# Performance work log

Measured on AMD Instinct MI355X. Metric: run time of the kernel, lower is better.

Reference implementation:

```python
import jax, jax.numpy as jnp
import numpy as np

B, N, H, SD, MAXS, MINS = 16, 1024, 64, 64, 16, 2
ETA = 0.01

def setup_inputs() -> dict:
    key = jax.random.key(0)
    ks = jax.random.split(key, 8)
    rn = lambda k, shape, sc=1.0: jax.random.normal(k, shape, dtype=jnp.float32) * sc
    return {
        "gene_state": rn(ks[0], (B, N, H)),
        "coherent_state": rn(ks[1], (B, N, H)),
        "state_embeddings": rn(ks[2], (MAXS, SD), 0.1),
        "gamma_base": jnp.ones((N,), jnp.float32) * 0.1,
        "env_w1": rn(ks[3], (H, 32), 0.1), "env_b1": jnp.zeros((32,), jnp.float32),
        "env_w2": rn(ks[4], (32, 1), 0.1), "env_b2": jnp.zeros((1,), jnp.float32),
        "omega_w1": rn(ks[5], (H, 32), 0.1), "omega_b1": jnp.zeros((32,), jnp.float32),
        "omega_w2": rn(ks[6], (32, 1), 0.1), "omega_b2": jnp.zeros((1,), jnp.float32),
        "Hmat": rn(ks[7], (N, N), 0.1),
    }

def reference(gene_state, coherent_state, state_embeddings, gamma_base,
              env_w1, env_b1, env_w2, env_b2,
              omega_w1, omega_b1, omega_w2, omega_b2, Hmat):
    # --- CellularStateBank: cosine-similarity softmax over active states ---
    cell = gene_state.mean(axis=1)                                   # [B, H]
    active = state_embeddings[:MINS]                                 # [MINS, SD]
    cn = cell / jnp.clip(jnp.linalg.norm(cell, axis=-1, keepdims=True), 1e-12)
    sn = active / jnp.clip(jnp.linalg.norm(active, axis=-1, keepdims=True), 1e-12)
    state_probs = jax.nn.softmax(cn @ sn.T / 0.1, axis=-1)           # [B, MINS]

    # --- DecoherenceLayer: env-coupled collapse toward classical mean ---
    h1 = jax.nn.silu(gene_state @ env_w1 + env_b1)                   # [B, N, 32]
    env = jax.nn.sigmoid((h1 @ env_w2 + env_b2)[..., 0])             # [B, N]
    gamma = jax.nn.sigmoid(gamma_base) * (1.0 + env)                 # [B, N]
    classical = jnp.mean(gene_state, axis=-1, keepdims=True)         # [B, N, 1]
    ge = gamma[..., None]
    decohered = (1.0 - ge) * coherent_state + ge * classical         # [B, N, H]

    # --- GreensFunctionLayer: batched complex resolvent inversion ---
    o1 = jax.nn.silu(gene_state @ omega_w1 + omega_b1)               # [B, N, 32]
    omega = (o1 @ omega_w2 + omega_b2)[..., 0]                       # [B, N]
    omega_mean = omega.mean(axis=1)                                  # [B]
    H_sym = 0.5 * (Hmat + Hmat.T)
    I = jnp.eye(N, dtype=jnp.complex64)
    w = omega_mean.astype(jnp.complex64) + jnp.complex64(1j * ETA)   # [B]
    R = w[:, None, None] * I - H_sym.astype(jnp.complex64)           # [B, N, N]
    propagator = jnp.abs(jnp.linalg.inv(R))                          # [B, N, N]

    return state_probs, decohered, gamma, propagator
```

## Files before the change

kernel.cpp:

```cpp
#include <hip/hip_runtime.h>
#include <hip/hip_bf16.h>

constexpr int kB  = 16;
constexpr int kN  = 1024;
constexpr int kH  = 64;
constexpr int kNB = 64;
constexpr int kNT = 16;

typedef float f4 __attribute__((ext_vector_type(4)));

__device__ __forceinline__ float2 cmul(float2 a, float2 b) {
  return make_float2(a.x * b.x - a.y * b.y, a.x * b.y + a.y * b.x);
}
__device__ __forceinline__ float2 cfma(float2 a, float2 b, float2 acc) {
  acc.x = fmaf(a.x, b.x, fmaf(-a.y, b.y, acc.x));
  acc.y = fmaf(a.x, b.y, fmaf( a.y, b.x, acc.y));
  return acc;
}
__device__ __forceinline__ float2 cnfma(float2 a, float2 b, float2 acc) {
  acc.x = fmaf(-a.x, b.x, fmaf( a.y, b.y, acc.x));
  acc.y = fmaf(-a.x, b.y, fmaf(-a.y, b.x, acc.y));
  return acc;
}
__device__ __forceinline__ float2 cinv(float2 p) {
  float d = 1.0f / (p.x * p.x + p.y * p.y);
  return make_float2(p.x * d, -p.y * d);
}
__device__ __forceinline__ float2 csel(bool c, float2 a, float2 b) {
  return c ? a : b;
}

struct TileLds {
  f4 Ar[64][9];
  f4 Ai[64][9];
  f4 Br[32][17];
  f4 Bi[32][17];
};

struct PivSmem {
  float2 P[kNB][kNB + 1];
  float2 Cst[kNB][4];
  float2 Rst[4][kNB];
};

union FusedSmem {
  TileLds tile;
  PivSmem piv;
};

union UpdSmem {
  TileLds tile;
  float2  M[64][66];
};

__device__ __forceinline__ void stage_tiles(
    TileLds& L, int t,
    const float* __restrict__ Agr, const float* __restrict__ Agi, int astride,
    const float* __restrict__ Bgr, const float* __restrict__ Bgi, int bstride)
{
  #pragma unroll
  for (int q = 0; q < 2; ++q) {
    int e = q * 256 + t;
    int ra = e >> 3, ca = e & 7;
    L.Ar[ra][ca] = *(const f4*)(Agr + (size_t)ra * astride + ca * 4);
    L.Ai[ra][ca] = *(const f4*)(Agi + (size_t)ra * astride + ca * 4);
    int rb = e >> 4, cb = e & 15;
    L.Br[rb][cb] = *(const f4*)(Bgr + (size_t)rb * bstride + cb * 4);
    L.Bi[rb][cb] = *(const f4*)(Bgi + (size_t)rb * bstride + cb * 4);
  }
}

__device__ __forceinline__ void prefetch_regs(
    int t,
    const float* __restrict__ Agr, const float* __restrict__ Agi, int astride,
    const float* __restrict__ Bgr, const float* __restrict__ Bgi, int bstride,
    f4 (&sar)[2], f4 (&sai)[2], f4 (&sbr)[2], f4 (&sbi)[2])
{
  #pragma unroll
  for (int q = 0; q < 2; ++q) {
    int e = q * 256 + t;
    int ra = e >> 3, ca = e & 7;
    sar[q] = *(const f4*)(Agr + (size_t)ra * astride + ca * 4);
    sai[q] = *(const f4*)(Agi + (size_t)ra * astride + ca * 4);
    int rb = e >> 4, cb = e & 15;
    sbr[q] = *(const f4*)(Bgr + (size_t)rb * bstride + cb * 4);
    sbi[q] = *(const f4*)(Bgi + (size_t)rb * bstride + cb * 4);
  }
}

__device__ __forceinline__ void regs_to_lds(
    TileLds& L, int t,
    const f4 (&sar)[2], const f4 (&sai)[2],
    const f4 (&sbr)[2], const f4 (&sbi)[2])
{
  #pragma unroll
  for (int q = 0; q < 2; ++q) {
    int e = q * 256 + t;
    int ra = e >> 3, ca = e & 7;
    L.Ar[ra][ca] = sar[q]; L.Ai[ra][ca] = sai[q];
    int rb = e >> 4, cb = e & 15;
    L.Br[rb][cb] = sbr[q]; L.Bi[rb][cb] = sbi[q];
  }
}

__device__ __forceinline__ void cgemm_tile(
    const TileLds& L, int r0, int c0q, float (&cr)[4][4], float (&ci)[4][4])
{
  #pragma unroll 2
  for (int mq = 0; mq < 8; ++mq) {
    f4 ar[4], ai[4];
    #pragma unroll
    for (int i = 0; i < 4; ++i) {
      ar[i] = L.Ar[r0 + i][mq];
      ai[i] = L.Ai[r0 + i][mq];
    }
    #pragma unroll
    for (int mm = 0; mm < 4; ++mm) {
      f4 br = L.Br[mq * 4 + mm][c0q];
      f4 bi = L.Bi[mq * 4 + mm][c0q];
      #pragma unroll
      for (int i = 0; i < 4; ++i) {
        float a_r = ar[i][mm], a_i = ai[i][mm];
        #pragma unroll
        for (int j = 0; j < 4; ++j) {
          cr[i][j] = fmaf(a_r, br[j], fmaf(-a_i, bi[j], cr[i][j]));
          ci[i][j] = fmaf(a_r, bi[j], fmaf( a_i, br[j], ci[i][j]));
        }
      }
    }
  }
}

__global__ __launch_bounds__(64) void rows_kernel(
    const float* __restrict__ gene, const float* __restrict__ coh,
    const float* __restrict__ gbase,
    const float* __restrict__ ew1, const float* __restrict__ eb1,
    const float* __restrict__ ew2, const float* __restrict__ eb2,
    const float* __restrict__ ow1, const float* __restrict__ ob1,
    const float* __restrict__ ow2, const float* __restrict__ ob2,
    float* __restrict__ out_dec, float* __restrict__ out_gamma,
    float* __restrict__ ws_omega)
{
  int row = blockIdx.x;
  int n   = row & (kN - 1);
  int t   = threadIdx.x;
  float g = gene[(size_t)row * kH + t];

  float s = g;
  #pragma unroll
  for (int off = 32; off >= 1; off >>= 1) s += __shfl_xor(s, off);
  float classical = s * (1.0f / kH);

  bool isEnv = t < 32;
  int  j     = isEnv ? t : (t - 32);
  const float* w1 = isEnv ? ew1 : ow1;
  float acc = isEnv ? eb1[j] : ob1[j];
  #pragma unroll
  for (int h = 0; h < kH; ++h) {
    float gh = __shfl(g, h);
    acc = fmaf(gh, w1[h * 32 + j], acc);
  }
  float sl   = acc * (1.0f / (1.0f + expf(-acc)));
  float term = sl * (isEnv ? ew2[j] : ow2[j]);
  #pragma unroll
  for (int off = 16; off >= 1; off >>= 1) term += __shfl_xor(term, off);
  float env_sum = __shfl(term, 0);
  float om_sum  = __shfl(term, 32);

  float env   = 1.0f / (1.0f + expf(-(env_sum + eb2[0])));
  float gamma = (1.0f / (1.0f + expf(-gbase[n]))) * (1.0f + env);

  float dec = (1.0f - gamma) * coh[(size_t)row * kH + t] + gamma * classical;
  out_dec[(size_t)row * kH + t] = dec;
  if (t == 0)  out_gamma[row] = gamma;
  if (t == 63) ws_omega[row]  = om_sum + ob2[0];
}

__global__ __launch_bounds__(256) void probs_kernel(
    const float* __restrict__ gene, const float* __restrict__ emb,
    float* __restrict__ outp)
{
  __shared__ float red[256];
  __shared__ float cell[64];
  int b = blockIdx.x, t = threadIdx.x;
  int h = t & 63, seg = t >> 6;
  float s = 0.0f;
  for (int n = seg * 256; n < seg * 256 + 256; ++n)
    s += gene[((size_t)b * kN + n) * kH + h];
  red[t] = s;
  __syncthreads();
  if (t < 64) cell[t] = (red[t] + red[t + 64] + red[t + 128] + red[t + 192]) * (1.0f / kN);
  __syncthreads();
  if (t == 0) {
    float nc = 0.0f;
    for (int x = 0; x < 64; ++x) nc += cell[x] * cell[x];
    nc = fmaxf(sqrtf(nc), 1e-12f);
    float l[2];
    for (int s2 = 0; s2 < 2; ++s2) {
      float ne = 0.0f, dot = 0.0f;
      for (int x = 0; x < 64; ++x) { float e = emb[s2 * 64 + x]; ne += e * e; }
      ne = fmaxf(sqrtf(ne), 1e-12f);
      for (int x = 0; x < 64; ++x) dot += (cell[x] / nc) * (emb[s2 * 64 + x] / ne);
      l[s2] = dot * 10.0f;
    }
    float m  = fmaxf(l[0], l[1]);
    float e0 = expf(l[0] - m), e1 = expf(l[1] - m);
    outp[b * 2 + 0] = e0 / (e0 + e1);
    outp[b * 2 + 1] = e1 / (e0 + e1);
  }
}

__global__ __launch_bounds__(256) void omean_kernel(
    const float* __restrict__ om, float* __restrict__ omm)
{
  __shared__ float red[256];
  int b = blockIdx.x, t = threadIdx.x;
  float s = om[b * kN + t] + om[b * kN + t + 256] + om[b * kN + t + 512] + om[b * kN + t + 768];
  red[t] = s;
  __syncthreads();
  for (int off = 128; off >= 1; off >>= 1) {
    if (t < off) red[t] += red[t + off];
    __syncthreads();
  }
  if (t == 0) omm[b] = red[0] * (1.0f / kN);
}

__global__ __launch_bounds__(256) void hs_kernel(
    const float* __restrict__ Hm, float* __restrict__ Hs)
{
  int idx = blockIdx.x * 256 + threadIdx.x;
  int i = idx >> 10, j = idx & 1023;
  Hs[idx] = 0.5f * (Hm[i * kN + j] + Hm[j * kN + i]);
}

__global__ __launch_bounds__(256) void build_kernel(
    const float* __restrict__ Hs, const float* __restrict__ omm,
    float* __restrict__ Are, float* __restrict__ Aim, int b0)
{
  int bb = blockIdx.y;
  int e = blockIdx.x * 256 + threadIdx.x;
  int i = e >> 8, j4 = e & 255;
  float wr = omm[b0 + bb];
  f4 h = *(const f4*)(Hs + (size_t)e * 4);
  f4 re, im;
  #pragma unroll
  for (int c = 0; c < 4; ++c) {
    bool d = (j4 * 4 + c == i);
    re[c] = (d ? wr : 0.0f) - h[c];
    im[c] = d ? 0.01f : 0.0f;
  }
  *(f4*)(Are + (size_t)bb * kN * kN + (size_t)e * 4) = re;
  *(f4*)(Aim + (size_t)bb * kN * kN + (size_t)e * 4) = im;
}

__device__ void pivotinv_dev(
    PivSmem& S,
    const float* __restrict__ Are, const float* __restrict__ Aim,
    float* __restrict__ Pro, float* __restrict__ Pio, int kstep, int bb, int t)
{
  size_t base = (size_t)bb * kN * kN + (size_t)(kstep * kNB) * kN + kstep * kNB;

  #pragma unroll
  for (int q = 0; q < 16; ++q) {
    int e = q * 256 + t;
    int r = e >> 6, c = e & 63;
    S.P[r][c] = make_float2(Are[base + (size_t)r * kN + c],
                            Aim[base + (size_t)r * kN + c]);
  }
  __syncthreads();

  const int c = t & 63;
  const int w = t >> 6;
  const int cq = c & 3;

  for (int ps = 0; ps < 16; ++ps) {
    const int p0 = ps * 4;
    S.Cst[t >> 2][t & 3]  = S.P[t >> 2][p0 + (t & 3)];
    S.Rst[t >> 6][t & 63] = S.P[p0 + (t >> 6)][t & 63];
    __syncthreads();

    float2 E[4][4];
    #pragma unroll
    for (int r = 0; r < 4; ++r)
      #pragma unroll
      for (int q = 0; q < 4; ++q) E[r][q] = S.Rst[r][p0 + q];
    #pragma unroll
    for (int s4 = 0; s4 < 4; ++s4) {
      float2 ip = cinv(E[s4][s4]);
      #pragma unroll
      for (int cc = 0; cc < 4; ++cc)
        if (cc != s4) E[s4][cc] = cmul(E[s4][cc], ip);
      #pragma unroll
      for (int i = 0; i < 4; ++i)
        if (i != s4) {
          float2 f = E[i][s4];
          #pragma unroll
          for (int cc = 0; cc < 4; ++cc)
            if (cc != s4) E[i][cc] = cnfma(f, E[s4][cc], E[i][cc]);
          E[i][s4] = cmul(make_float2(-f.x, -f.y), ip);
        }
      E[s4][s4] = ip;
    }

    float2 Rp[4];
    #pragma unroll
    for (int r = 0; r < 4; ++r) {
      float2 acc = cmul(E[r][0], S.Rst[0][c]);
      acc = cfma(E[r][1], S.Rst[1][c], acc);
      acc = cfma(E[r][2], S.Rst[2][c], acc);
      acc = cfma(E[r][3], S.Rst[3][c], acc);
      Rp[r] = acc;
    }

    const bool cinP = (c >= p0) && (c < p0 + 4);
    float2 Ecol[4];
    #pragma unroll
    for (int r = 0; r < 4; ++r) {
      float2 a = csel(cq & 1, E[r][1], E[r][0]);
      float2 b = csel(cq & 1, E[r][3], E[r][2]);
      Ecol[r] = csel(cq & 2, b, a);
    }
    float2 ra  = csel(w & 1, Rp[1], Rp[0]);
    float2 rb  = csel(w & 1, Rp[3], Rp[2]);
    float2 Rpw = csel(w & 2, rb, ra);
    float2 ea  = csel(w & 1, Ecol[1], Ecol[0]);
    float2 eb  = csel(w & 1, Ecol[3], Ecol[2]);
    float2 Ecw = csel(w & 2, eb, ea);
    float2 inPval = csel(cinP, Ecw, Rpw);

    #pragma unroll
    for (int qq = 0; qq < 16; ++qq) {
      int i = w + 4 * qq;
      const f4* fp = (const f4*)(&S.Cst[i][0]);
      f4 f01 = fp[0], f23 = fp[1];
      float2 f0 = make_float2(f01.x, f01.y), f1 = make_float2(f01.z, f01.w);
      float2 f2 = make_float2(f23.x, f23.y), f3 = make_float2(f23.z, f23.w);
      float2 old = S.P[i][c];
      float2 g = old;
      g = cnfma(f0, Rp[0], g);
      g = cnfma(f1, Rp[1], g);
      g = cnfma(f2, Rp[2], g);
      g = cnfma(f3, Rp[3], g);
      float2 cp = cmul(f0, Ecol[0]);
      cp = cfma(f1, Ecol[1], cp);
      cp = cfma(f2, Ecol[2], cp);
      cp = cfma(f3, Ecol[3], cp);
      cp.x = -cp.x; cp.y = -cp.y;
      float2 other = csel(cinP, cp, g);
      float2 res   = csel(qq == ps, inPval, other);
      S.P[i][c] = res;
    }
    __syncthreads();
  }

  int pbase = bb * kNB * kNB;
  #pragma unroll
  for (int q = 0; q < 16; ++q) {
    int e = q * 256 + t;
    int r = e >> 6, cc = e & 63;
    float2 v  = S.P[r][cc];
    float2 vt = S.P[cc][r];
    Pro[pbase + e] = 0.5f * (v.x + vt.x);
    Pio[pbase + e] = 0.5f * (v.y + vt.y);
  }
}

__global__ __launch_bounds__(256) void pivotinv_kernel(
    const float* __restrict__ Are, const float* __restrict__ Aim,
    float* __restrict__ Pro, float* __restrict__ Pio, int kstep)
{
  __shared__ PivSmem S;
  pivotinv_dev(S, Are, Aim, Pro, Pio, kstep, blockIdx.x, threadIdx.x);
}

__device__ void rowfix_dev(
    TileLds& L,
    float* __restrict__ Are, float* __restrict__ Aim,
    const float* __restrict__ Pr, const float* __restrict__ Pi,
    int kstep, int ct, int bb, int t)
{
  int pbase = bb * kNB * kNB;
  size_t rb = (size_t)bb * kN * kN + (size_t)(kstep * kNB) * kN + ct * kNB;
  if (ct == kstep) {
    for (int e = t; e < kNB * kNB / 4; e += 256) {
      int r = e >> 4, c4 = e & 15;
      *(f4*)(Are + rb + (size_t)r * kN + c4 * 4) = *(const f4*)(Pr + pbase + e * 4);
      *(f4*)(Aim + rb + (size_t)r * kN + c4 * 4) = *(const f4*)(Pi + pbase + e * 4);
    }
    return;
  }
  float cr[4][4] = {}, ci[4][4] = {};
  int r0 = (t >> 4) * 4, c0q = t & 15;

  stage_tiles(L, t, Pr + pbase, Pi + pbase, kNB,
              Are + rb, Aim + rb, kN);
  __syncthreads();

  f4 sar[2], sai[2], sbr[2], sbi[2];
  prefetch_regs(t, Pr + pbase + 32, Pi + pbase + 32, kNB,
                Are + rb + (size_t)32 * kN, Aim + rb + (size_t)32 * kN, kN,
                sar, sai, sbr, sbi);
  cgemm_tile(L, r0, c0q, cr, ci);
  __syncthreads();

  regs_to_lds(L, t, sar, sai, sbr, sbi);
  __syncthreads();
  cgemm_tile(L, r0, c0q, cr, ci);

  #pragma unroll
  for (int i = 0; i < 4; ++i) {
    size_t idx = rb + (size_t)(r0 + i) * kN + c0q * 4;
    *(f4*)(Are + idx) = (f4){cr[i][0], cr[i][1], cr[i][2], cr[i][3]};
    *(f4*)(Aim + idx) = (f4){ci[i][0], ci[i][1], ci[i][2], ci[i][3]};
  }
}

__global__ __launch_bounds__(256) void rowpiv_kernel(
    float* __restrict__ Are, float* __restrict__ Aim,
    const float* __restrict__ Prc, const float* __restrict__ Pic,
    float* __restrict__ Prn, float* __restrict__ Pin, int kstep)
{
  __shared__ FusedSmem S;
  int x = blockIdx.x, bb = blockIdx.y, t = threadIdx.x;
  if (x == kNT) {
    pivotinv_dev(S.piv, Are, Aim, Prn, Pin, kstep + 1, bb, t);
    return;
  }
  rowfix_dev(S.tile, Are, Aim, Prc, Pic, kstep, x, bb, t);
}

__global__ __launch_bounds__(256) void colgemm_kernel(
    float* __restrict__ Are, float* __restrict__ Aim,
    const float* __restrict__ Pr, const float* __restrict__ Pi, int kstep)
{
  int rt = blockIdx.x;
  if (rt == kstep) return;
  int bb = blockIdx.y, t = threadIdx.x;
  size_t abase = (size_t)bb * kN * kN + (size_t)(rt * kNB) * kN + kstep * kNB;
  int pbase = bb * kNB * kNB;
  __shared__ TileLds L;
  float cr[4][4] = {}, ci[4][4] = {};
  int r0 = (t >> 4) * 4, c0q = t & 15;

  stage_tiles(L, t, Are + abase, Aim + abase, kN,
              Pr + pbase, Pi + pbase, kNB);
  __syncthreads();

  f4 sar[2], sai[2], sbr[2], sbi[2];
  prefetch_regs(t, Are + abase + 32, Aim + abase + 32, kN,
                Pr + pbase + 32 * kNB, Pi + pbase + 32 * kNB, kNB,
                sar, sai, sbr, sbi);
  cgemm_tile(L, r0, c0q, cr, ci);
  __syncthreads();

  regs_to_lds(L, t, sar, sai, sbr, sbi);
  __syncthreads();
  cgemm_tile(L, r0, c0q, cr, ci);

  #pragma unroll
  for (int i = 0; i < 4; ++i) {
    size_t idx = abase + (size_t)(r0 + i) * kN + c0q * 4;
    *(f4*)(Are + idx) = (f4){-cr[i][0], -cr[i][1], -cr[i][2], -cr[i][3]};
    *(f4*)(Aim + idx) = (f4){-ci[i][0], -ci[i][1], -ci[i][2], -ci[i][3]};
  }
}

__global__ __launch_bounds__(256) void update_kernel(
    float* __restrict__ Are, float* __restrict__ Aim, int kstep)
{
  int idx = blockIdx.x;
  int bb  = blockIdx.y;
  int t   = threadIdx.x;
  int a = (int)((sqrtf(8.0f * (float)idx + 1.0f) - 1.0f) * 0.5f);
  while ((a + 1) * (a + 2) / 2 <= idx) ++a;
  while (a * (a + 1) / 2 > idx) --a;
  int b = idx - a * (a + 1) / 2;
  int rt = a + (a >= kstep);
  int ct = b + (b >= kstep);

  size_t NNb     = (size_t)bb * kN * kN;
  size_t colbase = NNb + (size_t)(rt * kNB) * kN + kstep * kNB;
  size_t rowbase = NNb + (size_t)(kstep * kNB) * kN + ct * kNB;
  size_t cb      = NNb + (size_t)(rt * kNB) * kN + ct * kNB;
  __shared__ UpdSmem S;
  float cr[4][4] = {}, ci[4][4] = {};
  int r0 = (t >> 4) * 4, c0q = t & 15;

  stage_tiles(S.tile, t, Are + colbase, Aim + colbase, kN,
              Are + rowbase, Aim + rowbase, kN);
  __syncthreads();

  f4 sar[2], sai[2], sbr[2], sbi[2];
  prefetch_regs(t, Are + colbase + 32, Aim + colbase + 32, kN,
                Are + rowbase + (size_t)32 * kN,
                Aim + rowbase + (size_t)32 * kN, kN,
                sar, sai, sbr, sbi);
  cgemm_tile(S.tile, r0, c0q, cr, ci);
  __syncthreads();

  regs_to_lds(S.tile, t, sar, sai, sbr, sbi);
  __syncthreads();
  cgemm_tile(S.tile, r0, c0q, cr, ci);

  f4 vr4[4], vi4[4];
  #pragma unroll
  for (int i = 0; i < 4; ++i) {
    size_t gidx = cb + (size_t)(r0 + i) * kN + c0q * 4;
    f4 vr = *(const f4*)(Are + gidx);
    f4 vi = *(const f4*)(Aim + gidx);
    vr += (f4){cr[i][0], cr[i][1], cr[i][2], cr[i][3]};
    vi += (f4){ci[i][0], ci[i][1], ci[i][2], ci[i][3]};
    *(f4*)(Are + gidx) = vr;
    *(f4*)(Aim + gidx) = vi;
    vr4[i] = vr; vi4[i] = vi;
  }

  if (rt != ct) {
    float eps = ((rt < kstep) == (ct < kstep)) ? 1.0f : -1.0f;
    __syncthreads();
    #pragma unroll
    for (int i = 0; i < 4; ++i)
      #pragma unroll
      for (int j = 0; j < 4; ++j)
        S.M[c0q * 4 + j][r0 + i] =
            make_float2(eps * vr4[i][j], eps * vi4[i][j]);
    __syncthreads();
    size_t mb = NNb + (size_t)(ct * kNB) * kN + rt * kNB;
    #pragma unroll
    for (int q = 0; q < 4; ++q) {
      int e = q * 256 + t;
      int r = e >> 4, c4 = e & 15;
      float2 m0 = S.M[r][c4 * 4 + 0], m1 = S.M[r][c4 * 4 + 1];
      float2 m2 = S.M[r][c4 * 4 + 2], m3 = S.M[r][c4 * 4 + 3];
      *(f4*)(Are + mb + (size_t)r * kN + c4 * 4) = (f4){m0.x, m1.x, m2.x, m3.x};
      *(f4*)(Aim + mb + (size_t)r * kN + c4 * 4) = (f4){m0.y, m1.y, m2.y, m3.y};
    }
  }
}

__global__ __launch_bounds__(256) void abs_kernel(
    const float* __restrict__ Are, const float* __restrict__ Aim,
    float* __restrict__ outp)
{
  size_t e = (size_t)blockIdx.x * 256 + threadIdx.x;
  f4 re = *(const f4*)(Are + e * 4);
  f4 im = *(const f4*)(Aim + e * 4);
  f4 o;
  #pragma unroll
  for (int c = 0; c < 4; ++c) o[c] = sqrtf(re[c] * re[c] + im[c] * im[c]);
  *(f4*)(outp + e * 4) = o;
}

extern "C" void kernel_launch(void* const* d_in, const int* in_sizes, int n_in,
                              void* d_out, int out_size, void* d_ws, size_t ws_size,
                              hipStream_t stream)
{
  const float* gene  = (const float*)d_in[0];
  const float* coh   = (const float*)d_in[1];
  const float* emb   = (const float*)d_in[2];
  const float* gbase = (const float*)d_in[3];
  const float* ew1   = (const float*)d_in[4];
  const float* eb1   = (const float*)d_in[5];
  const float* ew2   = (const float*)d_in[6];
  const float* eb2   = (const float*)d_in[7];
  const float* ow1   = (const float*)d_in[8];
  const float* ob1   = (const float*)d_in[9];
  const float* ow2   = (const float*)d_in[10];
  const float* ob2   = (const float*)d_in[11];
  const float* Hm    = (const float*)d_in[12];

  float* out       = (float*)d_out;
  float* out_probs = out;
  float* out_dec   = out + 32;
  float* out_gamma = out + 32 + 1048576;
  float* out_prop  = out + 32 + 1048576 + 16384;

  const size_t NN      = (size_t)kN * kN;
  const size_t PB      = (size_t)kNB * kNB;
  const size_t perB    = 2 * NN + 4 * PB;
  const size_t fixedF  = NN + (size_t)kB * kN + 16;
  size_t availF = ws_size / 4;
  int chunk = 1;
  if (availF > fixedF + perB) {
    size_t c = (availF - fixedF) / perB;
    chunk = (int)(c > 16 ? 16 : c);
    if (chunk < 1) chunk = 1;
  }

  float* Are  = (float*)d_ws;
  float* Aim  = Are + (size_t)chunk * NN;
  float* Pr0  = Aim + (size_t)chunk * NN;
  float* Pi0  = Pr0 + (size_t)chunk * PB;
  float* Pr1  = Pi0 + (size_t)chunk * PB;
  float* Pi1  = Pr1 + (size_t)chunk * PB;
  float* Hs   = Pi1 + (size_t)chunk * PB;
  float* wsom = Hs  + NN;
  float* womm = wsom + (size_t)kB * kN;

  rows_kernel<<<kB * kN, 64, 0, stream>>>(gene, coh, gbase, ew1, eb1, ew2, eb2,
                                          ow1, ob1, ow2, ob2,
                                          out_dec, out_gamma, wsom);
  probs_kernel<<<kB, 256, 0, stream>>>(gene, emb, out_probs);
  omean_kernel<<<kB, 256, 0, stream>>>(wsom, womm);
  hs_kernel<<<(kN * kN) / 256, 256, 0, stream>>>(Hm, Hs);

  for (int b0 = 0; b0 < kB; b0 += chunk) {
    int c = (b0 + chunk <= kB) ? chunk : (kB - b0);
    build_kernel<<<dim3((kN * kN) / 1024, c), 256, 0, stream>>>(Hs, womm, Are, Aim, b0);
    pivotinv_kernel<<<c, 256, 0, stream>>>(Are, Aim, Pr0, Pi0, 0);
    for (int k = 0; k < kNT; ++k) {
      float* Prc = (k & 1) ? Pr1 : Pr0;
      float* Pic = (k & 1) ? Pi1 : Pi0;
      float* Prn = (k & 1) ? Pr0 : Pr1;
      float* Pin = (k & 1) ? Pi0 : Pi1;
      colgemm_kernel<<<dim3(kNT, c), 256, 0, stream>>>(Are, Aim, Prc, Pic, k);
      update_kernel<<<dim3(120, c), 256, 0, stream>>>(Are, Aim, k);
      int gx = (k < kNT - 1) ? (kNT + 1) : kNT;
      rowpiv_kernel<<<dim3(gx, c), 256, 0, stream>>>(Are, Aim, Prc, Pic, Prn, Pin, k);
    }
    abs_kernel<<<c * (kN * kN / 1024), 256, 0, stream>>>(
        Are, Aim, out_prop + (size_t)b0 * NN);
  }
}
```

Before: 2.359 ms.

## Overlap next pivot inversion with trailing update and split probs reduction

Restructures the blocked Gauss-Jordan step schedule. The diagonal-tile update for the next pivot now runs first in its own tiny kernel. The next pivot-block inversion is then fused into the trailing-update launch, with its pair index skipped, so it runs concurrently with the bulk update rather than alongside the row fix. Row fixing becomes its own kernel. Separately, the per-batch cell mean reduction is split into a 16-way parallel partial-sum kernel plus a small finalize kernel to use more CUs. This adds one launch per step and an extra workspace buffer.

Result: slower. 3.199 ms (+35.6%).

```diff
diff --git a/kernel.cpp b/kernel.cpp
--- a/kernel.cpp
+++ b/kernel.cpp
@@ -43,14 +43,10 @@
   float2 Rst[4][kNB];
 };
 
-union FusedSmem {
-  TileLds tile;
-  PivSmem piv;
-};
-
-union UpdSmem {
+union UpdPivSmem {
   TileLds tile;
   float2  M[64][66];
+  PivSmem piv;
 };
 
 __device__ __forceinline__ void stage_tiles(
@@ -176,20 +172,32 @@
   if (t == 63) ws_omega[row]  = om_sum + ob2[0];
 }
 
-__global__ __launch_bounds__(256) void probs_kernel(
-    const float* __restrict__ gene, const float* __restrict__ emb,
+__global__ __launch_bounds__(256) void probs1_kernel(
+    const float* __restrict__ gene, float* __restrict__ prt)
+{
+  __shared__ float red[256];
+  int b = blockIdx.x, s = blockIdx.y, t = threadIdx.x;
+  int h = t & 63, q = t >> 6;
+  const float* gp = gene + ((size_t)b * kN + s * 64 + q * 16) * kH + h;
+  float sum = 0.0f;
+  #pragma unroll
+  for (int i = 0; i < 16; ++i) sum += gp[(size_t)i * kH];
+  red[t] = sum;
+  __syncthreads();
+  if (t < 64)
+    prt[(b * 16 + s) * 64 + t] = red[t] + red[t + 64] + red[t + 128] + red[t + 192];
+}
+
+__global__ __launch_bounds__(64) void probs2_kernel(
+    const float* __restrict__ prt, const float* __restrict__ emb,
     float* __restrict__ outp)
 {
-  __shared__ float red[256];
   __shared__ float cell[64];
   int b = blockIdx.x, t = threadIdx.x;
-  int h = t & 63, seg = t >> 6;
   float s = 0.0f;
-  for (int n = seg * 256; n < seg * 256 + 256; ++n)
-    s += gene[((size_t)b * kN + n) * kH + h];
-  red[t] = s;
-  __syncthreads();
-  if (t < 64) cell[t] = (red[t] + red[t + 64] + red[t + 128] + red[t + 192]) * (1.0f / kN);
+  #pragma unroll
+  for (int i = 0; i < 16; ++i) s += prt[(b * 16 + i) * 64 + t];
+  cell[t] = s * (1.0f / kN);
   __syncthreads();
   if (t == 0) {
     float nc = 0.0f;
@@ -373,62 +381,6 @@
   pivotinv_dev(S, Are, Aim, Pro, Pio, kstep, blockIdx.x, threadIdx.x);
 }
 
-__device__ void rowfix_dev(
-    TileLds& L,
-    float* __restrict__ Are, float* __restrict__ Aim,
-    const float* __restrict__ Pr, const float* __restrict__ Pi,
-    int kstep, int ct, int bb, int t)
-{
-  int pbase = bb * kNB * kNB;
-  size_t rb = (size_t)bb * kN * kN + (size_t)(kstep * kNB) * kN + ct * kNB;
-  if (ct == kstep) {
-    for (int e = t; e < kNB * kNB / 4; e += 256) {
-      int r = e >> 4, c4 = e & 15;
-      *(f4*)(Are + rb + (size_t)r * kN + c4 * 4) = *(const f4*)(Pr + pbase + e * 4);
-      *(f4*)(Aim + rb + (size_t)r * kN + c4 * 4) = *(const f4*)(Pi + pbase + e * 4);
-    }
-    return;
-  }
-  float cr[4][4] = {}, ci[4][4] = {};
-  int r0 = (t >> 4) * 4, c0q = t & 15;
-
-  stage_tiles(L, t, Pr + pbase, Pi + pbase, kNB,
-              Are + rb, Aim + rb, kN);
-  __syncthreads();
-
-  f4 sar[2], sai[2], sbr[2], sbi[2];
-  prefetch_regs(t, Pr + pbase + 32, Pi + pbase + 32, kNB,
-                Are + rb + (size_t)32 * kN, Aim + rb + (size_t)32 * kN, kN,
-                sar, sai, sbr, sbi);
-  cgemm_tile(L, r0, c0q, cr, ci);
-  __syncthreads();
-
-  regs_to_lds(L, t, sar, sai, sbr, sbi);
-  __syncthreads();
-  cgemm_tile(L, r0, c0q, cr, ci);
-
-  #pragma unroll
-  for (int i = 0; i < 4; ++i) {
-    size_t idx = rb + (size_t)(r0 + i) * kN + c0q * 4;
-    *(f4*)(Are + idx) = (f4){cr[i][0], cr[i][1], cr[i][2], cr[i][3]};
-    *(f4*)(Aim + idx) = (f4){ci[i][0], ci[i][1], ci[i][2], ci[i][3]};
-  }
-}
-
-__global__ __launch_bounds__(256) void rowpiv_kernel(
-    float* __restrict__ Are, float* __restrict__ Aim,
-    const float* __restrict__ Prc, const float* __restrict__ Pic,
-    float* __restrict__ Prn, float* __restrict__ Pin, int kstep)
-{
-  __shared__ FusedSmem S;
-  int x = blockIdx.x, bb = blockIdx.y, t = threadIdx.x;
-  if (x == kNT) {
-    pivotinv_dev(S.piv, Are, Aim, Prn, Pin, kstep + 1, bb, t);
-    return;
-  }
-  rowfix_dev(S.tile, Are, Aim, Prc, Pic, kstep, x, bb, t);
-}
-
 __global__ __launch_bounds__(256) void colgemm_kernel(
     float* __restrict__ Are, float* __restrict__ Aim,
     const float* __restrict__ Pr, const float* __restrict__ Pi, int kstep)
@@ -465,12 +417,10 @@
   }
 }
 
-__global__ __launch_bounds__(256) void update_kernel(
-    float* __restrict__ Are, float* __restrict__ Aim, int kstep)
-{
-  int idx = blockIdx.x;
-  int bb  = blockIdx.y;
-  int t   = threadIdx.x;
+__device__ void update_pair_dev(
+    UpdPivSmem& S, float* __restrict__ Are, float* __restrict__ Aim,
+    int kstep, int idx, int bb, int t)
+{
   int a = (int)((sqrtf(8.0f * (float)idx + 1.0f) - 1.0f) * 0.5f);
   while ((a + 1) * (a + 2) / 2 <= idx) ++a;
   while (a * (a + 1) / 2 > idx) --a;
@@ -482,7 +432,6 @@
   size_t colbase = NNb + (size_t)(rt * kNB) * kN + kstep * kNB;
   size_t rowbase = NNb + (size_t)(kstep * kNB) * kN + ct * kNB;
   size_t cb      = NNb + (size_t)(rt * kNB) * kN + ct * kNB;
-  __shared__ UpdSmem S;
   float cr[4][4] = {}, ci[4][4] = {};
   int r0 = (t >> 4) * 4, c0q = t & 15;
 
@@ -535,6 +484,71 @@
       *(f4*)(Are + mb + (size_t)r * kN + c4 * 4) = (f4){m0.x, m1.x, m2.x, m3.x};
       *(f4*)(Aim + mb + (size_t)r * kN + c4 * 4) = (f4){m0.y, m1.y, m2.y, m3.y};
     }
+  }
+}
+
+__global__ __launch_bounds__(256) void updiag_kernel(
+    float* __restrict__ Are, float* __restrict__ Aim, int kstep)
+{
+  __shared__ UpdPivSmem S;
+  int idxd = kstep * (kstep + 1) / 2 + kstep;
+  update_pair_dev(S, Are, Aim, kstep, idxd, blockIdx.y, threadIdx.x);
+}
+
+__global__ __launch_bounds__(256) void updpiv_kernel(
+    float* __restrict__ Are, float* __restrict__ Aim,
+    float* __restrict__ Prn, float* __restrict__ Pin,
+    int kstep, int skipidx, int withpiv)
+{
+  __shared__ UpdPivSmem S;
+  int x = blockIdx.x, bb = blockIdx.y, t = threadIdx.x;
+  if (withpiv && x == (int)gridDim.x - 1) {
+    pivotinv_dev(S.piv, Are, Aim, Prn, Pin, kstep + 1, bb, t);
+    return;
+  }
+  int idx = x + ((skipidx >= 0 && x >= skipidx) ? 1 : 0);
+  update_pair_dev(S, Are, Aim, kstep, idx, bb, t);
+}
+
+__global__ __launch_bounds__(256) void rowfix_kernel(
+    float* __restrict__ Are, float* __restrict__ Aim,
+    const float* __restrict__ Pr, const float* __restrict__ Pi, int kstep)
+{
+  int ct = blockIdx.x, bb = blockIdx.y, t = threadIdx.x;
+  int pbase = bb * kNB * kNB;
+  size_t rb = (size_t)bb * kN * kN + (size_t)(kstep * kNB) * kN + ct * kNB;
+  if (ct == kstep) {
+    for (int e = t; e < kNB * kNB / 4; e += 256) {
+      int r = e >> 4, c4 = e & 15;
+      *(f4*)(Are + rb + (size_t)r * kN + c4 * 4) = *(const f4*)(Pr + pbase + e * 4);
+      *(f4*)(Aim + rb + (size_t)r * kN + c4 * 4) = *(const f4*)(Pi + pbase + e * 4);
+    }
+    return;
+  }
+  __shared__ TileLds L;
+  float cr[4][4] = {}, ci[4][4] = {};
+  int r0 = (t >> 4) * 4, c0q = t & 15;
+
+  stage_tiles(L, t, Pr + pbase, Pi + pbase, kNB,
+              Are + rb, Aim + rb, kN);
+  __syncthreads();
+
+  f4 sar[2], sai[2], sbr[2], sbi[2];
+  prefetch_regs(t, Pr + pbase + 32, Pi + pbase + 32, kNB,
+                Are + rb + (size_t)32 * kN, Aim + rb + (size_t)32 * kN, kN,
+                sar, sai, sbr, sbi);
+  cgemm_tile(L, r0, c0q, cr, ci);
+  __syncthreads();
+
+  regs_to_lds(L, t, sar, sai, sbr, sbi);
+  __syncthreads();
+  cgemm_tile(L, r0, c0q, cr, ci);
+
+  #pragma unroll
+  for (int i = 0; i < 4; ++i) {
+    size_t idx = rb + (size_t)(r0 + i) * kN + c0q * 4;
+    *(f4*)(Are + idx) = (f4){cr[i][0], cr[i][1], cr[i][2], cr[i][3]};
+    *(f4*)(Aim + idx) = (f4){ci[i][0], ci[i][1], ci[i][2], ci[i][3]};
   }
 }
 
@@ -578,7 +592,7 @@
   const size_t NN      = (size_t)kN * kN;
   const size_t PB      = (size_t)kNB * kNB;
   const size_t perB    = 2 * NN + 4 * PB;
-  const size_t fixedF  = NN + (size_t)kB * kN + 16;
+  const size_t fixedF  = NN + (size_t)kB * kN + 16 + (size_t)kB * 16 * 64;
   size_t availF = ws_size / 4;
   int chunk = 1;
   if (availF > fixedF + perB) {
@@ -596,11 +610,13 @@
   float* Hs   = Pi1 + (size_t)chunk * PB;
   float* wsom = Hs  + NN;
   float* womm = wsom + (size_t)kB * kN;
+  float* prt  = womm + 16;
 
   rows_kernel<<<kB * kN, 64, 0, stream>>>(gene, coh, gbase, ew1, eb1, ew2, eb2,
                                           ow1, ob1, ow2, ob2,
                                           out_dec, out_gamma, wsom);
-  probs_kernel<<<kB, 256, 0, stream>>>(gene, emb, out_probs);
+  probs1_kernel<<<dim3(kB, 16), 256, 0, stream>>>(gene, prt);
+  probs2_kernel<<<kB, 64, 0, stream>>>(prt, emb, out_probs);
   omean_kernel<<<kB, 256, 0, stream>>>(wsom, womm);
   hs_kernel<<<(kN * kN) / 256, 256, 0, stream>>>(Hm, Hs);
 
@@ -614,9 +630,16 @@
       float* Prn = (k & 1) ? Pr0 : Pr1;
       float* Pin = (k & 1) ? Pi0 : Pi1;
       colgemm_kernel<<<dim3(kNT, c), 256, 0, stream>>>(Are, Aim, Prc, Pic, k);
-      update_kernel<<<dim3(120, c), 256, 0, stream>>>(Are, Aim, k);
-      int gx = (k < kNT - 1) ? (kNT + 1) : kNT;
-      rowpiv_kernel<<<dim3(gx, c), 256, 0, stream>>>(Are, Aim, Prc, Pic, Prn, Pin, k);
+      if (k < kNT - 1) {
+        int skip = k * (k + 1) / 2 + k;
+        updiag_kernel<<<dim3(1, c), 256, 0, stream>>>(Are, Aim, k);
+        updpiv_kernel<<<dim3(120, c), 256, 0, stream>>>(Are, Aim, Prn, Pin,
+                                                        k, skip, 1);
+      } else {
+        updpiv_kernel<<<dim3(120, c), 256, 0, stream>>>(Are, Aim, Prn, Pin,
+                                                        k, -1, 0);
+      }
+      rowfix_kernel<<<dim3(kNT, c), 256, 0, stream>>>(Are, Aim, Prc, Pic, k);
     }
     abs_kernel<<<c * (kN * kN / 1024), 256, 0, stream>>>(
         Are, Aim, out_prop + (size_t)b0 * NN);
```
